# Optimization experiments

Hardware: AMD Instinct MI355X
Metric: run time of the kernel (lower is better)

The kernel has to match this reference:

```python
import jax, jax.numpy as jnp
import numpy as np

N_HEAD = 16
N_STATE = 1024
NEG_INF = -1e9


def setup_inputs() -> dict:
    key = jax.random.key(0)
    k1, = jax.random.split(key, 1)
    B, S = 4, 2048
    x = jax.random.normal(k1, (B, S, 3 * N_STATE), dtype=jnp.float32)
    # causal attention mask (1 = keep, 0 = masked), broadcast over heads
    attn_mask = jnp.tril(jnp.ones((S, S), dtype=jnp.float32))[None, None, :, :]
    attn_mask = jnp.broadcast_to(attn_mask, (B, 1, S, S))
    return {"x": x, "attn_mask": attn_mask}


def reference(x, attn_mask) -> jnp.ndarray:
    B, S, _ = x.shape
    d_head = N_STATE // N_HEAD
    q = x[:, :, :N_STATE].reshape(B, S, N_HEAD, d_head).transpose(0, 2, 1, 3)  # [B,H,S,D]
    k = x[:, :, N_STATE:2 * N_STATE].reshape(B, S, N_HEAD, d_head).transpose(0, 2, 1, 3)
    v = x[:, :, 2 * N_STATE:].reshape(B, S, N_HEAD, d_head).transpose(0, 2, 1, 3)
    scale = 1.0 / jnp.sqrt(jnp.asarray(d_head, dtype=x.dtype))
    w = jnp.einsum('bhqd,bhkd->bhqk', q, k) * scale           # [B,H,S,S]
    w = attn_mask * w + (1.0 - attn_mask) * NEG_INF
    w = jax.nn.softmax(w, axis=-1)
    # attention_dropout is identity at inference (Keras Dropout, training=False)
    a = jnp.einsum('bhqk,bhkd->bhqd', w, v)                   # [B,H,S,D]
    return a.transpose(0, 2, 1, 3).reshape(B, S, N_STATE)
```

## Files before the change

### kernel.cpp

```cpp
#include <hip/hip_runtime.h>


typedef float  f32x4  __attribute__((ext_vector_type(4)));
typedef short  bf16x8 __attribute__((ext_vector_type(8)));
typedef short  bf16x4 __attribute__((ext_vector_type(4)));

#define NH      16
#define DH      64
#define SEQ     2048
#define NSTATE  1024
#define ROW3    3072
#define BQ      128
#define BK      64
#define NQB     (SEQ / BQ)
#define KST     72
#define VST     68
#define PST     72
#define NEG_BIG (-1e9f)

static __device__ __forceinline__ short f2bf(float f) {
    unsigned u = __builtin_bit_cast(unsigned, f);
    u += 0x7FFFu + ((u >> 16) & 1u);
    return (short)(u >> 16);
}

__global__ __launch_bounds__(512, 4)
void mha_fwd(const float* __restrict__ x, float* __restrict__ out) {
    const int tid  = threadIdx.x;
    const int wave = tid >> 6;
    const int lane = tid & 63;
    const int l16  = lane & 15;
    const int quad = lane >> 4;

    const int pr = blockIdx.x;
    const int bh = blockIdx.y;
    const int b  = bh >> 4;
    const int h  = bh & 15;

    const float* xb    = x + (size_t)b * SEQ * ROW3;
    const float* kbase = xb + NSTATE + h * DH;
    const float* vbase = xb + 2 * NSTATE + h * DH;
    float*       ob    = out + (size_t)b * SEQ * NSTATE + h * DH;

    __shared__ short Klds[BK * KST];
    __shared__ short Vlds[DH * VST];
    __shared__ short Plds[8][16 * PST];

#pragma unroll 1
    for (int ph = 0; ph < 2; ++ph) {
        const int qblk = ph ? (NQB - 1 - pr) : pr;
        const int q0   = qblk * BQ;
        const int qmin = q0 + wave * 16;
        const int qrow = qmin + l16;

        bf16x8 qf[2];
        {
            const float* qp = xb + (size_t)qrow * ROW3 + h * DH + quad * 8;
#pragma unroll
            for (int f = 0; f < 2; ++f) {
                float4 a = *(const float4*)(qp + 32 * f);
                float4 c = *(const float4*)(qp + 32 * f + 4);
                bf16x8 v;
                v[0] = f2bf(a.x * 0.125f); v[1] = f2bf(a.y * 0.125f);
                v[2] = f2bf(a.z * 0.125f); v[3] = f2bf(a.w * 0.125f);
                v[4] = f2bf(c.x * 0.125f); v[5] = f2bf(c.y * 0.125f);
                v[6] = f2bf(c.z * 0.125f); v[7] = f2bf(c.w * 0.125f);
                qf[f] = v;
            }
        }

        f32x4 o[4];
#pragma unroll
        for (int t = 0; t < 4; ++t) o[t] = (f32x4){0.f, 0.f, 0.f, 0.f};
        float m_run = -3e38f;
        float l_run = 0.f;

        const int ntiles = q0 / BK + BQ / BK;
        for (int it = 0; it < ntiles; ++it) {
            const int kv0 = it * BK;
            __syncthreads();

#pragma unroll
            for (int i = 0; i < 4; ++i) {
                int p  = tid + 512 * i;
                int kv = p >> 5;
                int d  = (p & 31) * 2;
                const float* gp = kbase + (size_t)(kv0 + kv) * ROW3 + d;
                float2 v = *(const float2*)gp;
                unsigned pk = (unsigned)(unsigned short)f2bf(v.x) |
                              ((unsigned)(unsigned short)f2bf(v.y) << 16);
                *(unsigned*)&Klds[kv * KST + d] = pk;
            }
#pragma unroll
            for (int i = 0; i < 4; ++i) {
                int idx = tid + 512 * i;
                int d   = idx & 63;
                int kv  = (idx >> 6) * 2;
                const float* gp = vbase + (size_t)(kv0 + kv) * ROW3 + d;
                float v0 = gp[0];
                float v1 = gp[ROW3];
                unsigned pk = (unsigned)(unsigned short)f2bf(v0) |
                              ((unsigned)(unsigned short)f2bf(v1) << 16);
                *(unsigned*)&Vlds[d * VST + kv] = pk;
            }
            __syncthreads();

            if (kv0 > qmin + 15) continue;

            bf16x8 kf[4][2];
#pragma unroll
            for (int t = 0; t < 4; ++t)
#pragma unroll
                for (int f = 0; f < 2; ++f)
                    kf[t][f] = *(const bf16x8*)&Klds[(16 * t + l16) * KST + quad * 8 + 32 * f];
            bf16x8 vf[4][2];
#pragma unroll
            for (int t = 0; t < 4; ++t)
#pragma unroll
                for (int f = 0; f < 2; ++f) {
                    bf16x4 lo = *(const bf16x4*)&Vlds[(16 * t + l16) * VST + quad * 8 + 32 * f];
                    bf16x4 hi = *(const bf16x4*)&Vlds[(16 * t + l16) * VST + quad * 8 + 32 * f + 4];
                    vf[t][f] = __builtin_shufflevector(lo, hi, 0, 1, 2, 3, 4, 5, 6, 7);
                }

            f32x4 sc[4];
#pragma unroll
            for (int t = 0; t < 4; ++t) {
                f32x4 c = (f32x4){0.f, 0.f, 0.f, 0.f};
                c = __builtin_amdgcn_mfma_f32_16x16x32_bf16(kf[t][0], qf[0], c, 0, 0, 0);
                c = __builtin_amdgcn_mfma_f32_16x16x32_bf16(kf[t][1], qf[1], c, 0, 0, 0);
                sc[t] = c;
            }
            if (kv0 + BK - 1 > qmin) {
#pragma unroll
                for (int t = 0; t < 4; ++t)
#pragma unroll
                    for (int r = 0; r < 4; ++r) {
                        int kvg = kv0 + 16 * t + 4 * quad + r;
                        if (kvg > qrow) sc[t][r] = NEG_BIG;
                    }
            }

            float vmax = sc[0][0];
#pragma unroll
            for (int t = 0; t < 4; ++t)
#pragma unroll
                for (int r = 0; r < 4; ++r) vmax = fmaxf(vmax, sc[t][r]);
            vmax = fmaxf(vmax, __shfl_xor(vmax, 16));
            vmax = fmaxf(vmax, __shfl_xor(vmax, 32));
            const float mnew  = fmaxf(m_run, vmax);
            const float alpha = __expf(m_run - mnew);
            m_run = mnew;
            float lsum = 0.f;
#pragma unroll
            for (int t = 0; t < 4; ++t)
#pragma unroll
                for (int r = 0; r < 4; ++r) {
                    float pv = __expf(sc[t][r] - mnew);
                    sc[t][r] = pv;
                    lsum += pv;
                }
            lsum += __shfl_xor(lsum, 16);
            lsum += __shfl_xor(lsum, 32);
            l_run = l_run * alpha + lsum;

            short* pb = &Plds[wave][0];
#pragma unroll
            for (int t = 0; t < 4; ++t) {
                bf16x4 pk;
                pk[0] = f2bf(sc[t][0]); pk[1] = f2bf(sc[t][1]);
                pk[2] = f2bf(sc[t][2]); pk[3] = f2bf(sc[t][3]);
                *(bf16x4*)&pb[l16 * PST + 16 * t + 4 * quad] = pk;
            }
            __asm__ volatile("s_waitcnt lgkmcnt(0)" ::: "memory");
            bf16x8 pf0 = *(const bf16x8*)&pb[l16 * PST + quad * 8];
            bf16x8 pf1 = *(const bf16x8*)&pb[l16 * PST + quad * 8 + 32];

            float ar[4];
#pragma unroll
            for (int r = 0; r < 4; ++r) ar[r] = __shfl(alpha, 4 * quad + r);
#pragma unroll
            for (int t = 0; t < 4; ++t) {
                f32x4 c = o[t];
#pragma unroll
                for (int r = 0; r < 4; ++r) c[r] *= ar[r];
                c = __builtin_amdgcn_mfma_f32_16x16x32_bf16(pf0, vf[t][0], c, 0, 0, 0);
                c = __builtin_amdgcn_mfma_f32_16x16x32_bf16(pf1, vf[t][1], c, 0, 0, 0);
                o[t] = c;
            }
        }

        {
            float linv = 1.0f / l_run;
            float lr[4];
#pragma unroll
            for (int r = 0; r < 4; ++r) lr[r] = __shfl(linv, 4 * quad + r);
            const int qtop = qmin + 4 * quad;
#pragma unroll
            for (int t = 0; t < 4; ++t)
#pragma unroll
                for (int r = 0; r < 4; ++r)
                    ob[(size_t)(qtop + r) * NSTATE + 16 * t + l16] = o[t][r] * lr[r];
        }
    }
}

extern "C" void kernel_launch(void* const* d_in, const int* in_sizes, int n_in,
                              void* d_out, int out_size, void* d_ws, size_t ws_size,
                              hipStream_t stream) {
    const float* x = (const float*)d_in[0];
    float* out = (float*)d_out;
    dim3 grid(NQB / 2, 4 * NH);
    dim3 block(512);
    hipLaunchKernelGGL(mha_fwd, grid, block, 0, stream, x, out);
}
```

Before: 269.6 us.

## Stage 128-key KV tiles per sync, use exp2 softmax and packed bf16 conversion

The shared-memory staging tile for K and V grows from 64 to 128 keys, and each staged tile is processed as two 64-key sub-tiles. This halves the number of barrier pairs per query block and lets the K loads use float4. The softmax now folds log2(e) into the Q scale and uses exp2f instead of __expf. bf16 packing uses a perm builtin that packs two values at once. In exchange, shared memory use grows, which can lower occupancy, and waves whose causal range ends early sit idle while the tile is staged.

```diff
diff --git a/kernel.cpp b/kernel.cpp
--- a/kernel.cpp
+++ b/kernel.cpp
@@ -3,7 +3,6 @@
 
 typedef float  f32x4  __attribute__((ext_vector_type(4)));
 typedef short  bf16x8 __attribute__((ext_vector_type(8)));
-typedef short  bf16x4 __attribute__((ext_vector_type(4)));
 
 #define NH      16
 #define DH      64
@@ -11,17 +10,20 @@
 #define NSTATE  1024
 #define ROW3    3072
 #define BQ      128
-#define BK      64
+#define BKS     128
 #define NQB     (SEQ / BQ)
 #define KST     72
-#define VST     68
+#define VST     132
 #define PST     72
 #define NEG_BIG (-1e9f)
-
-static __device__ __forceinline__ short f2bf(float f) {
-    unsigned u = __builtin_bit_cast(unsigned, f);
-    u += 0x7FFFu + ((u >> 16) & 1u);
-    return (short)(u >> 16);
+#define QSC     (0.125f * 1.4426950408889634f)
+
+static __device__ __forceinline__ unsigned pk2(float x, float y) {
+    unsigned ux = __builtin_bit_cast(unsigned, x);
+    unsigned uy = __builtin_bit_cast(unsigned, y);
+    ux += 0x7FFFu + ((ux >> 16) & 1u);
+    uy += 0x7FFFu + ((uy >> 16) & 1u);
+    return __builtin_amdgcn_perm(uy, ux, 0x07060302u);
 }
 
 __global__ __launch_bounds__(512, 4)
@@ -42,7 +44,7 @@
     const float* vbase = xb + 2 * NSTATE + h * DH;
     float*       ob    = out + (size_t)b * SEQ * NSTATE + h * DH;
 
-    __shared__ short Klds[BK * KST];
+    __shared__ short Klds[BKS * KST];
     __shared__ short Vlds[DH * VST];
     __shared__ short Plds[8][16 * PST];
 
@@ -60,12 +62,12 @@
             for (int f = 0; f < 2; ++f) {
                 float4 a = *(const float4*)(qp + 32 * f);
                 float4 c = *(const float4*)(qp + 32 * f + 4);
-                bf16x8 v;
-                v[0] = f2bf(a.x * 0.125f); v[1] = f2bf(a.y * 0.125f);
-                v[2] = f2bf(a.z * 0.125f); v[3] = f2bf(a.w * 0.125f);
-                v[4] = f2bf(c.x * 0.125f); v[5] = f2bf(c.y * 0.125f);
-                v[6] = f2bf(c.z * 0.125f); v[7] = f2bf(c.w * 0.125f);
-                qf[f] = v;
+                union { bf16x8 v; unsigned u[4]; } qq;
+                qq.u[0] = pk2(a.x * QSC, a.y * QSC);
+                qq.u[1] = pk2(a.z * QSC, a.w * QSC);
+                qq.u[2] = pk2(c.x * QSC, c.y * QSC);
+                qq.u[3] = pk2(c.z * QSC, c.w * QSC);
+                qf[f] = qq.v;
             }
         }
 
@@ -75,118 +77,126 @@
         float m_run = -3e38f;
         float l_run = 0.f;
 
-        const int ntiles = q0 / BK + BQ / BK;
-        for (int it = 0; it < ntiles; ++it) {
-            const int kv0 = it * BK;
+        const int nst = q0 / BKS + 1;
+#pragma unroll 1
+        for (int st = 0; st < nst; ++st) {
+            const int kvb = st * BKS;
             __syncthreads();
 
 #pragma unroll
             for (int i = 0; i < 4; ++i) {
                 int p  = tid + 512 * i;
-                int kv = p >> 5;
-                int d  = (p & 31) * 2;
-                const float* gp = kbase + (size_t)(kv0 + kv) * ROW3 + d;
-                float2 v = *(const float2*)gp;
-                unsigned pk = (unsigned)(unsigned short)f2bf(v.x) |
-                              ((unsigned)(unsigned short)f2bf(v.y) << 16);
-                *(unsigned*)&Klds[kv * KST + d] = pk;
-            }
-#pragma unroll
-            for (int i = 0; i < 4; ++i) {
+                int kv = p >> 4;
+                int d  = (p & 15) * 4;
+                const float* gp = kbase + (size_t)(kvb + kv) * ROW3 + d;
+                float4 v = *(const float4*)gp;
+                uint2 pk;
+                pk.x = pk2(v.x, v.y);
+                pk.y = pk2(v.z, v.w);
+                *(uint2*)&Klds[kv * KST + d] = pk;
+            }
+#pragma unroll
+            for (int i = 0; i < 8; ++i) {
                 int idx = tid + 512 * i;
                 int d   = idx & 63;
                 int kv  = (idx >> 6) * 2;
-                const float* gp = vbase + (size_t)(kv0 + kv) * ROW3 + d;
+                const float* gp = vbase + (size_t)(kvb + kv) * ROW3 + d;
                 float v0 = gp[0];
                 float v1 = gp[ROW3];
-                unsigned pk = (unsigned)(unsigned short)f2bf(v0) |
-                              ((unsigned)(unsigned short)f2bf(v1) << 16);
-                *(unsigned*)&Vlds[d * VST + kv] = pk;
+                *(unsigned*)&Vlds[d * VST + kv] = pk2(v0, v1);
             }
             __syncthreads();
 
-            if (kv0 > qmin + 15) continue;
-
-            bf16x8 kf[4][2];
-#pragma unroll
-            for (int t = 0; t < 4; ++t)
-#pragma unroll
-                for (int f = 0; f < 2; ++f)
-                    kf[t][f] = *(const bf16x8*)&Klds[(16 * t + l16) * KST + quad * 8 + 32 * f];
-            bf16x8 vf[4][2];
-#pragma unroll
-            for (int t = 0; t < 4; ++t)
-#pragma unroll
-                for (int f = 0; f < 2; ++f) {
-                    bf16x4 lo = *(const bf16x4*)&Vlds[(16 * t + l16) * VST + quad * 8 + 32 * f];
-                    bf16x4 hi = *(const bf16x4*)&Vlds[(16 * t + l16) * VST + quad * 8 + 32 * f + 4];
-                    vf[t][f] = __builtin_shufflevector(lo, hi, 0, 1, 2, 3, 4, 5, 6, 7);
-                }
-
-            f32x4 sc[4];
-#pragma unroll
-            for (int t = 0; t < 4; ++t) {
-                f32x4 c = (f32x4){0.f, 0.f, 0.f, 0.f};
-                c = __builtin_amdgcn_mfma_f32_16x16x32_bf16(kf[t][0], qf[0], c, 0, 0, 0);
-                c = __builtin_amdgcn_mfma_f32_16x16x32_bf16(kf[t][1], qf[1], c, 0, 0, 0);
-                sc[t] = c;
-            }
-            if (kv0 + BK - 1 > qmin) {
+#pragma unroll 1
+            for (int j = 0; j < 2; ++j) {
+                const int kv0 = kvb + 64 * j;
+                if (kv0 > qmin + 15) break;
+
+                bf16x8 kf[4][2];
+#pragma unroll
+                for (int t = 0; t < 4; ++t)
+#pragma unroll
+                    for (int f = 0; f < 2; ++f)
+                        kf[t][f] = *(const bf16x8*)
+                            &Klds[(64 * j + 16 * t + l16) * KST + quad * 8 + 32 * f];
+                bf16x8 vf[4][2];
+#pragma unroll
+                for (int t = 0; t < 4; ++t)
+#pragma unroll
+                    for (int f = 0; f < 2; ++f) {
+                        const short* vp = &Vlds[(16 * t + l16) * VST + 64 * j
+                                                + quad * 8 + 32 * f];
+                        typedef short bf16x4 __attribute__((ext_vector_type(4)));
+                        bf16x4 lo = *(const bf16x4*)vp;
+                        bf16x4 hi = *(const bf16x4*)(vp + 4);
+                        vf[t][f] = __builtin_shufflevector(lo, hi, 0,1,2,3,4,5,6,7);
+                    }
+
+                f32x4 sc[4];
+#pragma unroll
+                for (int t = 0; t < 4; ++t) {
+                    f32x4 c = (f32x4){0.f, 0.f, 0.f, 0.f};
+                    c = __builtin_amdgcn_mfma_f32_16x16x32_bf16(kf[t][0], qf[0], c, 0, 0, 0);
+                    c = __builtin_amdgcn_mfma_f32_16x16x32_bf16(kf[t][1], qf[1], c, 0, 0, 0);
+                    sc[t] = c;
+                }
+                if (kv0 + 63 > qmin) {
+#pragma unroll
+                    for (int t = 0; t < 4; ++t)
+#pragma unroll
+                        for (int r = 0; r < 4; ++r) {
+                            int kvg = kv0 + 16 * t + 4 * quad + r;
+                            if (kvg > qrow) sc[t][r] = NEG_BIG;
+                        }
+                }
+
+                float vmax = sc[0][0];
+#pragma unroll
+                for (int t = 0; t < 4; ++t)
+#pragma unroll
+                    for (int r = 0; r < 4; ++r) vmax = fmaxf(vmax, sc[t][r]);
+                vmax = fmaxf(vmax, __shfl_xor(vmax, 16));
+                vmax = fmaxf(vmax, __shfl_xor(vmax, 32));
+                const float mnew  = fmaxf(m_run, vmax);
+                const float alpha = exp2f(m_run - mnew);
+                m_run = mnew;
+                float lsum = 0.f;
 #pragma unroll
                 for (int t = 0; t < 4; ++t)
 #pragma unroll
                     for (int r = 0; r < 4; ++r) {
-                        int kvg = kv0 + 16 * t + 4 * quad + r;
-                        if (kvg > qrow) sc[t][r] = NEG_BIG;
+                        float pv = exp2f(sc[t][r] - mnew);
+                        sc[t][r] = pv;
+                        lsum += pv;
                     }
-            }
-
-            float vmax = sc[0][0];
-#pragma unroll
-            for (int t = 0; t < 4; ++t)
-#pragma unroll
-                for (int r = 0; r < 4; ++r) vmax = fmaxf(vmax, sc[t][r]);
-            vmax = fmaxf(vmax, __shfl_xor(vmax, 16));
-            vmax = fmaxf(vmax, __shfl_xor(vmax, 32));
-            const float mnew  = fmaxf(m_run, vmax);
-            const float alpha = __expf(m_run - mnew);
-            m_run = mnew;
-            float lsum = 0.f;
-#pragma unroll
-            for (int t = 0; t < 4; ++t)
-#pragma unroll
-                for (int r = 0; r < 4; ++r) {
-                    float pv = __expf(sc[t][r] - mnew);
-                    sc[t][r] = pv;
-                    lsum += pv;
-                }
-            lsum += __shfl_xor(lsum, 16);
-            lsum += __shfl_xor(lsum, 32);
-            l_run = l_run * alpha + lsum;
-
-            short* pb = &Plds[wave][0];
-#pragma unroll
-            for (int t = 0; t < 4; ++t) {
-                bf16x4 pk;
-                pk[0] = f2bf(sc[t][0]); pk[1] = f2bf(sc[t][1]);
-                pk[2] = f2bf(sc[t][2]); pk[3] = f2bf(sc[t][3]);
-                *(bf16x4*)&pb[l16 * PST + 16 * t + 4 * quad] = pk;
-            }
-            __asm__ volatile("s_waitcnt lgkmcnt(0)" ::: "memory");
-            bf16x8 pf0 = *(const bf16x8*)&pb[l16 * PST + quad * 8];
-            bf16x8 pf1 = *(const bf16x8*)&pb[l16 * PST + quad * 8 + 32];
-
-            float ar[4];
-#pragma unroll
-            for (int r = 0; r < 4; ++r) ar[r] = __shfl(alpha, 4 * quad + r);
-#pragma unroll
-            for (int t = 0; t < 4; ++t) {
-                f32x4 c = o[t];
-#pragma unroll
-                for (int r = 0; r < 4; ++r) c[r] *= ar[r];
-                c = __builtin_amdgcn_mfma_f32_16x16x32_bf16(pf0, vf[t][0], c, 0, 0, 0);
-                c = __builtin_amdgcn_mfma_f32_16x16x32_bf16(pf1, vf[t][1], c, 0, 0, 0);
-                o[t] = c;
+                lsum += __shfl_xor(lsum, 16);
+                lsum += __shfl_xor(lsum, 32);
+                l_run = l_run * alpha + lsum;
+
+                short* pb = &Plds[wave][0];
+#pragma unroll
+                for (int t = 0; t < 4; ++t) {
+                    uint2 pk;
+                    pk.x = pk2(sc[t][0], sc[t][1]);
+                    pk.y = pk2(sc[t][2], sc[t][3]);
+                    *(uint2*)&pb[l16 * PST + 16 * t + 4 * quad] = pk;
+                }
+                __asm__ volatile("s_waitcnt lgkmcnt(0)" ::: "memory");
+                bf16x8 pf0 = *(const bf16x8*)&pb[l16 * PST + quad * 8];
+                bf16x8 pf1 = *(const bf16x8*)&pb[l16 * PST + quad * 8 + 32];
+
+                float ar[4];
+#pragma unroll
+                for (int r = 0; r < 4; ++r) ar[r] = __shfl(alpha, 4 * quad + r);
+#pragma unroll
+                for (int t = 0; t < 4; ++t) {
+                    f32x4 c = o[t];
+#pragma unroll
+                    for (int r = 0; r < 4; ++r) c[r] *= ar[r];
+                    c = __builtin_amdgcn_mfma_f32_16x16x32_bf16(pf0, vf[t][0], c, 0, 0, 0);
+                    c = __builtin_amdgcn_mfma_f32_16x16x32_bf16(pf1, vf[t][1], c, 0, 0, 0);
+                    o[t] = c;
+                }
             }
         }
 
```

Result: no change. 270.8 us (+0.4%).
